# Optimization experiments

Measured on AMD Instinct MI355X. Metric: run time of the kernel, lower is better.

Reference implementation:

```python
import jax, jax.numpy as jnp
import numpy as np

B = 8192
NUM_SAMPLES = 128
RESAMPLE_PADDING = 0.01
F32_EPS = float(np.finfo(np.float32).eps)


def lift_gaussian_diag(d, t_mean, t_var, r_var):
    # d: [B,3]; t_mean/t_var/r_var: [B,S]
    mean = d[..., None, :] * t_mean[..., None]                      # [B,S,3]
    d_mag_sq = jnp.clip(jnp.sum(d ** 2, axis=-1, keepdims=True), 1e-10)
    d_outer_diag = d ** 2
    null_outer_diag = 1.0 - d_outer_diag / d_mag_sq
    cov_diag = (t_var[..., None] * d_outer_diag[..., None, :]
                + r_var[..., None] * null_outer_diag[..., None, :])  # [B,S,3]
    return mean, cov_diag


def conical_frustum_to_gaussian(d, t0, t1, base_radius):
    # stable=True branch of the original code
    mu = (t0 + t1) / 2
    hw = (t1 - t0) / 2
    t_mean = mu + 2 * mu * hw ** 2 / (3 * mu ** 2 + hw ** 2)
    t_var = hw ** 2 / 3 - 4 / 15 * (hw ** 4 * (12 * mu ** 2 - hw ** 2)
                                    / (3 * mu ** 2 + hw ** 2) ** 2)
    r_var = base_radius ** 2 * (mu ** 2 / 4 + 5 / 12 * hw ** 2
                                - 4 / 15 * hw ** 4 / (3 * mu ** 2 + hw ** 2))
    return lift_gaussian_diag(d, t_mean, t_var, r_var)


def cast_rays(t_vals, origins, directions, radii):
    # ray_shape == 'cone', diag == True
    means, covs = conical_frustum_to_gaussian(
        directions, t_vals[..., :-1], t_vals[..., 1:], radii)
    return means + origins[..., None, :], covs


def sorted_piecewise_constant_pdf(bins, weights, num_samples):
    # randomized=False branch; faithful O(n*m) mask-based interval search
    eps = 1e-5
    weight_sum = jnp.sum(weights, axis=-1, keepdims=True)
    padding = jnp.clip(eps - weight_sum, 0)
    weights = weights + padding / weights.shape[-1]
    weight_sum = weight_sum + padding
    pdf = weights / weight_sum
    cdf = jnp.minimum(jnp.cumsum(pdf[..., :-1], axis=-1), 1.0)
    z = jnp.zeros(cdf.shape[:-1] + (1,), cdf.dtype)
    o = jnp.ones(cdf.shape[:-1] + (1,), cdf.dtype)
    cdf = jnp.concatenate([z, cdf, o], axis=-1)                      # [B, nb+1]
    u = jnp.linspace(0.0, 1.0 - F32_EPS, num_samples, dtype=cdf.dtype)
    u = jnp.broadcast_to(u, cdf.shape[:-1] + (num_samples,))         # [B, S]
    mask = u[..., None, :] >= cdf[..., :, None]                      # [B, nb+1, S]

    def find_interval(x):
        x0 = jnp.max(jnp.where(mask, x[..., None], x[..., :1, None]), axis=-2)
        x1 = jnp.min(jnp.where(~mask, x[..., None], x[..., -1:, None]), axis=-2)
        return x0, x1

    bins_g0, bins_g1 = find_interval(bins)
    cdf_g0, cdf_g1 = find_interval(cdf)
    t = jnp.clip(jnp.nan_to_num((u - cdf_g0) / (cdf_g1 - cdf_g0)), 0, 1)
    return bins_g0 + t * (bins_g1 - bins_g0)


def setup_inputs() -> dict:
    key = jax.random.key(0)
    k0, k1, k2, k3 = jax.random.split(key, 4)
    origins = jax.random.normal(k0, (B, 3), dtype=jnp.float32)
    directions = jax.random.normal(k1, (B, 3), dtype=jnp.float32)
    directions = directions / jnp.linalg.norm(directions, axis=-1, keepdims=True)
    radii = 0.001 + 0.01 * jax.random.uniform(k2, (B, 1), dtype=jnp.float32)
    near = 2.0 * jnp.ones((B, 1), dtype=jnp.float32)
    far = 6.0 * jnp.ones((B, 1), dtype=jnp.float32)
    weights = jax.random.uniform(k3, (B, NUM_SAMPLES), dtype=jnp.float32)
    return {"origins": origins, "directions": directions, "radii": radii,
            "near": near, "far": far, "weights": weights}


def reference(origins, directions, radii, near, far, weights):
    # coarse stratified sampling (randomized=False, lindisp=False)
    t = jnp.linspace(0.0, 1.0, NUM_SAMPLES + 1, dtype=jnp.float32)
    t_coarse = near * (1.0 - t) + far * t                            # [B, S+1]
    means_c, covs_c = cast_rays(t_coarse, origins, directions, radii)
    # resample_along_rays: blur weights then inverse-CDF sample
    wpad = jnp.concatenate([weights[..., :1], weights, weights[..., -1:]], axis=-1)
    wmax = jnp.maximum(wpad[..., :-1], wpad[..., 1:])
    wblur = 0.5 * (wmax[..., :-1] + wmax[..., 1:]) + RESAMPLE_PADDING
    t_fine = sorted_piecewise_constant_pdf(t_coarse, wblur, t_coarse.shape[-1])
    means_f, covs_f = cast_rays(t_fine, origins, directions, radii)
    return (t_coarse, means_c, covs_c, t_fine, means_f, covs_f)
```

## Files before the change

kernel.cpp:

```cpp
#include <hip/hip_runtime.h>


constexpr int B_RAYS = 8192;
constexpr int S      = 128;
constexpr int SP1    = 129;
constexpr float F32_EPS = 1.1920928955078125e-07f;

constexpr long long O_TC = 0;
constexpr long long O_MC = O_TC + (long long)B_RAYS * SP1;
constexpr long long O_CC = O_MC + (long long)B_RAYS * S * 3;
constexpr long long O_TF = O_CC + (long long)B_RAYS * S * 3;
constexpr long long O_MF = O_TF + (long long)B_RAYS * SP1;
constexpr long long O_CF = O_MF + (long long)B_RAYS * S * 3;

__device__ __forceinline__ void cast_and_store(
    const float* __restrict__ sh_tv,
    float* __restrict__ sh_stage,
    float dx, float dy, float dz,
    float ox, float oy, float oz,
    float rad2, float dmag2,
    float* __restrict__ out_means,
    float* __restrict__ out_covs,
    int tid)
{
    float t0 = sh_tv[tid], t1 = sh_tv[tid + 1];
    float mu  = 0.5f * (t0 + t1);
    float hw  = 0.5f * (t1 - t0);
    float mu2 = mu * mu, hw2 = hw * hw, hw4 = hw2 * hw2;
    float den = 3.0f * mu2 + hw2;
    float t_mean = mu + (2.0f * mu * hw2) / den;
    float t_var  = hw2 * (1.0f / 3.0f)
                 - (4.0f / 15.0f) * ((hw4 * (12.0f * mu2 - hw2)) / (den * den));
    float r_var  = rad2 * (0.25f * mu2 + (5.0f / 12.0f) * hw2
                 - (4.0f / 15.0f) * (hw4 / den));

    float dxx = dx * dx, dyy = dy * dy, dzz = dz * dz;

    sh_stage[3 * tid + 0] = dx * t_mean + ox;
    sh_stage[3 * tid + 1] = dy * t_mean + oy;
    sh_stage[3 * tid + 2] = dz * t_mean + oz;
    sh_stage[384 + 3 * tid + 0] = t_var * dxx + r_var * (1.0f - dxx / dmag2);
    sh_stage[384 + 3 * tid + 1] = t_var * dyy + r_var * (1.0f - dyy / dmag2);
    sh_stage[384 + 3 * tid + 2] = t_var * dzz + r_var * (1.0f - dzz / dmag2);
    __syncthreads();
    #pragma unroll
    for (int j = 0; j < 3; ++j) {
        out_means[j * 128 + tid] = sh_stage[j * 128 + tid];
        out_covs [j * 128 + tid] = sh_stage[384 + j * 128 + tid];
    }
}

__global__ __launch_bounds__(128) void mipnerf_kernel(
    const float* __restrict__ origins,
    const float* __restrict__ directions,
    const float* __restrict__ radii,
    const float* __restrict__ nearp,
    const float* __restrict__ farp,
    const float* __restrict__ weights,
    float* __restrict__ out)
{
    const int b   = blockIdx.x;
    const int tid = threadIdx.x;

    __shared__ float sh_t[SP1];
    __shared__ float sh_tf[SP1];
    __shared__ float sh_cdf[SP1];
    __shared__ float sh_w[S];
    __shared__ float sh_stage[2 * S * 3];
    __shared__ float sh_red[2];
    __shared__ float sh_wavetot;

    const float ox = origins[3 * b], oy = origins[3 * b + 1], oz = origins[3 * b + 2];
    const float dx = directions[3 * b], dy = directions[3 * b + 1], dz = directions[3 * b + 2];
    const float rad  = radii[b];
    const float rad2 = rad * rad;
    const float nv = nearp[b], fv = farp[b];
    const float dmag2 = fmaxf(dx * dx + dy * dy + dz * dz, 1e-10f);

    for (int i = tid; i < SP1; i += 128) {
        float t  = (float)i * (1.0f / 128.0f);
        float tc = nv * (1.0f - t) + fv * t;
        sh_t[i] = tc;
        out[O_TC + (long long)b * SP1 + i] = tc;
    }
    sh_w[tid] = weights[(long long)b * S + tid];
    __syncthreads();

    cast_and_store(sh_t, sh_stage, dx, dy, dz, ox, oy, oz, rad2, dmag2,
                   out + O_MC + (long long)b * S * 3,
                   out + O_CC + (long long)b * S * 3, tid);

    float wi  = sh_w[tid];
    float wml = fmaxf((tid > 0     ? sh_w[tid - 1] : wi), wi);
    float wmr = fmaxf(wi, (tid < S - 1 ? sh_w[tid + 1] : wi));
    float wb  = 0.5f * (wml + wmr) + 0.01f;

    float v = wb;
    #pragma unroll
    for (int off = 32; off >= 1; off >>= 1) v += __shfl_down(v, off);
    if ((tid & 63) == 0) sh_red[tid >> 6] = v;
    __syncthreads();
    float wsum    = sh_red[0] + sh_red[1];
    float padding = fmaxf(1e-5f - wsum, 0.0f);
    float wstot   = wsum + padding;
    float pdf     = (wb + padding * (1.0f / (float)S)) / wstot;

    float x   = pdf;
    int lane  = tid & 63;
    #pragma unroll
    for (int off = 1; off < 64; off <<= 1) {
        float y = __shfl_up(x, off);
        if (lane >= off) x += y;
    }
    if (tid == 63) sh_wavetot = x;
    __syncthreads();
    if (tid >= 64) x += sh_wavetot;

    if (tid == 0) { sh_cdf[0] = 0.0f; sh_cdf[S] = 1.0f; }
    if (tid < S - 1) sh_cdf[tid + 1] = fminf(x, 1.0f);
    __syncthreads();

    const float ustep = (1.0f - F32_EPS) * (1.0f / 128.0f);
    for (int s = tid; s < SP1; s += 128) {
        float u = (float)s * ustep;
        int lo = 0, hi = S;
        #pragma unroll
        for (int it = 0; it < 7; ++it) {
            int mid = (lo + hi) >> 1;
            if (sh_cdf[mid] <= u) lo = mid; else hi = mid;
        }
        float cg0 = sh_cdf[lo], cg1 = sh_cdf[lo + 1];
        float bg0 = sh_t[lo],   bg1 = sh_t[lo + 1];
        float tt  = (u - cg0) / (cg1 - cg0);
        if (!(tt == tt)) tt = 0.0f;
        tt = fminf(fmaxf(tt, 0.0f), 1.0f);
        float tf = bg0 + tt * (bg1 - bg0);
        sh_tf[s] = tf;
        out[O_TF + (long long)b * SP1 + s] = tf;
    }
    __syncthreads();

    cast_and_store(sh_tf, sh_stage, dx, dy, dz, ox, oy, oz, rad2, dmag2,
                   out + O_MF + (long long)b * S * 3,
                   out + O_CF + (long long)b * S * 3, tid);
}

extern "C" void kernel_launch(void* const* d_in, const int* in_sizes, int n_in,
                              void* d_out, int out_size, void* d_ws, size_t ws_size,
                              hipStream_t stream)
{
    const float* origins    = (const float*)d_in[0];
    const float* directions = (const float*)d_in[1];
    const float* radii      = (const float*)d_in[2];
    const float* nearp      = (const float*)d_in[3];
    const float* farp       = (const float*)d_in[4];
    const float* weights    = (const float*)d_in[5];
    float* out = (float*)d_out;

    mipnerf_kernel<<<B_RAYS, 128, 0, stream>>>(
        origins, directions, radii, nearp, farp, weights, out);
}
```

Baseline: 21.30 us.

## Process one ray per wavefront, four rays per block, without block barriers

```diff
diff --git a/kernel.cpp b/kernel.cpp
--- a/kernel.cpp
+++ b/kernel.cpp
@@ -13,44 +13,26 @@
 constexpr long long O_MF = O_TF + (long long)B_RAYS * SP1;
 constexpr long long O_CF = O_MF + (long long)B_RAYS * S * 3;
 
-__device__ __forceinline__ void cast_and_store(
-    const float* __restrict__ sh_tv,
-    float* __restrict__ sh_stage,
-    float dx, float dy, float dz,
-    float ox, float oy, float oz,
-    float rad2, float dmag2,
-    float* __restrict__ out_means,
-    float* __restrict__ out_covs,
-    int tid)
+__device__ __forceinline__ void frustum(float t0, float t1, float rad2,
+                                        float& tm, float& tv, float& rv)
 {
-    float t0 = sh_tv[tid], t1 = sh_tv[tid + 1];
     float mu  = 0.5f * (t0 + t1);
     float hw  = 0.5f * (t1 - t0);
     float mu2 = mu * mu, hw2 = hw * hw, hw4 = hw2 * hw2;
     float den = 3.0f * mu2 + hw2;
-    float t_mean = mu + (2.0f * mu * hw2) / den;
-    float t_var  = hw2 * (1.0f / 3.0f)
-                 - (4.0f / 15.0f) * ((hw4 * (12.0f * mu2 - hw2)) / (den * den));
-    float r_var  = rad2 * (0.25f * mu2 + (5.0f / 12.0f) * hw2
-                 - (4.0f / 15.0f) * (hw4 / den));
-
-    float dxx = dx * dx, dyy = dy * dy, dzz = dz * dz;
-
-    sh_stage[3 * tid + 0] = dx * t_mean + ox;
-    sh_stage[3 * tid + 1] = dy * t_mean + oy;
-    sh_stage[3 * tid + 2] = dz * t_mean + oz;
-    sh_stage[384 + 3 * tid + 0] = t_var * dxx + r_var * (1.0f - dxx / dmag2);
-    sh_stage[384 + 3 * tid + 1] = t_var * dyy + r_var * (1.0f - dyy / dmag2);
-    sh_stage[384 + 3 * tid + 2] = t_var * dzz + r_var * (1.0f - dzz / dmag2);
-    __syncthreads();
-    #pragma unroll
-    for (int j = 0; j < 3; ++j) {
-        out_means[j * 128 + tid] = sh_stage[j * 128 + tid];
-        out_covs [j * 128 + tid] = sh_stage[384 + j * 128 + tid];
-    }
+    float rden = 1.0f / den;
+    tm = mu + (2.0f * mu * hw2) * rden;
+    tv = hw2 * (1.0f / 3.0f)
+       - (4.0f / 15.0f) * (hw4 * (12.0f * mu2 - hw2)) * (rden * rden);
+    rv = rad2 * (0.25f * mu2 + (5.0f / 12.0f) * hw2 - (4.0f / 15.0f) * hw4 * rden);
 }
 
-__global__ __launch_bounds__(128) void mipnerf_kernel(
+__device__ __forceinline__ float sel3(int c, float x, float y, float z)
+{
+    return (c == 0) ? x : ((c == 1) ? y : z);
+}
+
+__global__ __launch_bounds__(256) void mipnerf_kernel(
     const float* __restrict__ origins,
     const float* __restrict__ directions,
     const float* __restrict__ radii,
@@ -59,90 +41,124 @@
     const float* __restrict__ weights,
     float* __restrict__ out)
 {
-    const int b   = blockIdx.x;
     const int tid = threadIdx.x;
+    const int w   = tid >> 6;
+    const int l   = tid & 63;
+    const int b   = (blockIdx.x << 2) + w;
 
-    __shared__ float sh_t[SP1];
-    __shared__ float sh_tf[SP1];
-    __shared__ float sh_cdf[SP1];
-    __shared__ float sh_w[S];
-    __shared__ float sh_stage[2 * S * 3];
-    __shared__ float sh_red[2];
-    __shared__ float sh_wavetot;
+    __shared__ float s_tm[4][128];
+    __shared__ float s_tv[4][128];
+    __shared__ float s_rv[4][128];
+    __shared__ float s_cdf[4][132];
+    __shared__ float s_tf[4][132];
 
-    const float ox = origins[3 * b], oy = origins[3 * b + 1], oz = origins[3 * b + 2];
-    const float dx = directions[3 * b], dy = directions[3 * b + 1], dz = directions[3 * b + 2];
+    const float ox = origins[3*b+0], oy = origins[3*b+1], oz = origins[3*b+2];
+    const float dx = directions[3*b+0], dy = directions[3*b+1], dz = directions[3*b+2];
     const float rad  = radii[b];
     const float rad2 = rad * rad;
     const float nv = nearp[b], fv = farp[b];
-    const float dmag2 = fmaxf(dx * dx + dy * dy + dz * dz, 1e-10f);
+    const float dmag2 = fmaxf(dx*dx + dy*dy + dz*dz, 1e-10f);
+    const float axx = dx*dx, ayy = dy*dy, azz = dz*dz;
+    const float nxx = 1.0f - axx/dmag2, nyy = 1.0f - ayy/dmag2, nzz = 1.0f - azz/dmag2;
 
-    for (int i = tid; i < SP1; i += 128) {
-        float t  = (float)i * (1.0f / 128.0f);
-        float tc = nv * (1.0f - t) + fv * t;
-        sh_t[i] = tc;
-        out[O_TC + (long long)b * SP1 + i] = tc;
+    auto bin = [&](int k) {
+        float t = (float)k * (1.0f / 128.0f);
+        return nv * (1.0f - t) + fv * t;
+    };
+
+    auto write_cast = [&](float* __restrict__ om, float* __restrict__ oc) {
+        #pragma unroll
+        for (int j = 0; j < 3; ++j) {
+            int f0 = 2 * (l + 64*j);
+            int ia = f0 / 3,      ca = f0 - 3*ia;
+            int ib2 = (f0+1) / 3, cb = (f0+1) - 3*ib2;
+            float tma = s_tm[w][ia], tmb = s_tm[w][ib2];
+            float2 mv;
+            mv.x = sel3(ca, dx, dy, dz) * tma + sel3(ca, ox, oy, oz);
+            mv.y = sel3(cb, dx, dy, dz) * tmb + sel3(cb, ox, oy, oz);
+            *reinterpret_cast<float2*>(om + f0) = mv;
+            float2 cv;
+            cv.x = s_tv[w][ia] * sel3(ca, axx, ayy, azz)
+                 + s_rv[w][ia] * sel3(ca, nxx, nyy, nzz);
+            cv.y = s_tv[w][ib2] * sel3(cb, axx, ayy, azz)
+                 + s_rv[w][ib2] * sel3(cb, nxx, nyy, nzz);
+            *reinterpret_cast<float2*>(oc + f0) = cv;
+        }
+    };
+
+    for (int s = l; s < SP1; s += 64)
+        out[O_TC + (long long)b * SP1 + s] = bin(s);
+
+    #pragma unroll
+    for (int j = 0; j < 2; ++j) {
+        int i = l + 64*j;
+        float tm, tv, rv;
+        frustum(bin(i), bin(i+1), rad2, tm, tv, rv);
+        s_tm[w][i] = tm; s_tv[w][i] = tv; s_rv[w][i] = rv;
     }
-    sh_w[tid] = weights[(long long)b * S + tid];
-    __syncthreads();
+    __builtin_amdgcn_wave_barrier();
 
-    cast_and_store(sh_t, sh_stage, dx, dy, dz, ox, oy, oz, rad2, dmag2,
-                   out + O_MC + (long long)b * S * 3,
-                   out + O_CC + (long long)b * S * 3, tid);
+    write_cast(out + O_MC + (long long)b * 384, out + O_CC + (long long)b * 384);
+    __builtin_amdgcn_wave_barrier();
 
-    float wi  = sh_w[tid];
-    float wml = fmaxf((tid > 0     ? sh_w[tid - 1] : wi), wi);
-    float wmr = fmaxf(wi, (tid < S - 1 ? sh_w[tid + 1] : wi));
-    float wb  = 0.5f * (wml + wmr) + 0.01f;
+    float2 wv = *reinterpret_cast<const float2*>(weights + (long long)b * S + 2*l);
+    float wprev = __shfl_up(wv.y, 1);   if (l == 0)  wprev = wv.x;
+    float wnext = __shfl_down(wv.x, 1); if (l == 63) wnext = wv.y;
+    float m0 = fmaxf(wprev, wv.x), m1 = fmaxf(wv.x, wv.y), m2 = fmaxf(wv.y, wnext);
+    float wb0 = 0.5f * (m0 + m1) + 0.01f;
+    float wb1 = 0.5f * (m1 + m2) + 0.01f;
 
-    float v = wb;
-    #pragma unroll
-    for (int off = 32; off >= 1; off >>= 1) v += __shfl_down(v, off);
-    if ((tid & 63) == 0) sh_red[tid >> 6] = v;
-    __syncthreads();
-    float wsum    = sh_red[0] + sh_red[1];
-    float padding = fmaxf(1e-5f - wsum, 0.0f);
-    float wstot   = wsum + padding;
-    float pdf     = (wb + padding * (1.0f / (float)S)) / wstot;
-
-    float x   = pdf;
-    int lane  = tid & 63;
+    float ps   = wb0 + wb1;
+    float incl = ps;
     #pragma unroll
     for (int off = 1; off < 64; off <<= 1) {
-        float y = __shfl_up(x, off);
-        if (lane >= off) x += y;
+        float y = __shfl_up(incl, off);
+        if (l >= off) incl += y;
     }
-    if (tid == 63) sh_wavetot = x;
-    __syncthreads();
-    if (tid >= 64) x += sh_wavetot;
+    float total = __shfl(incl, 63);
+    float pad   = fmaxf(1e-5f - total, 0.0f);
+    float wstot = total + pad;
+    float inv   = 1.0f / wstot;
+    float padk  = pad * (1.0f / 128.0f);
+    float excl  = incl - ps;
 
-    if (tid == 0) { sh_cdf[0] = 0.0f; sh_cdf[S] = 1.0f; }
-    if (tid < S - 1) sh_cdf[tid + 1] = fminf(x, 1.0f);
-    __syncthreads();
+    float c1 = fminf((excl + wb0 + (float)(2*l + 1) * padk) * inv, 1.0f);
+    float c2 = fminf((incl        + (float)(2*l + 2) * padk) * inv, 1.0f);
+    s_cdf[w][2*l + 1] = c1;
+    s_cdf[w][2*l + 2] = (l == 63) ? 1.0f : c2;
+    if (l == 0) s_cdf[w][0] = 0.0f;
+    __builtin_amdgcn_wave_barrier();
 
     const float ustep = (1.0f - F32_EPS) * (1.0f / 128.0f);
-    for (int s = tid; s < SP1; s += 128) {
+    for (int s = l; s < SP1; s += 64) {
         float u = (float)s * ustep;
-        int lo = 0, hi = S;
+        int lo = 0, hi = 128;
         #pragma unroll
         for (int it = 0; it < 7; ++it) {
             int mid = (lo + hi) >> 1;
-            if (sh_cdf[mid] <= u) lo = mid; else hi = mid;
+            if (s_cdf[w][mid] <= u) lo = mid; else hi = mid;
         }
-        float cg0 = sh_cdf[lo], cg1 = sh_cdf[lo + 1];
-        float bg0 = sh_t[lo],   bg1 = sh_t[lo + 1];
-        float tt  = (u - cg0) / (cg1 - cg0);
+        float c0  = s_cdf[w][lo], cg1 = s_cdf[w][lo + 1];
+        float tt  = (u - c0) / (cg1 - c0);
         if (!(tt == tt)) tt = 0.0f;
         tt = fminf(fmaxf(tt, 0.0f), 1.0f);
-        float tf = bg0 + tt * (bg1 - bg0);
-        sh_tf[s] = tf;
+        float b0  = bin(lo);
+        float tf  = b0 + tt * (bin(lo + 1) - b0);
+        s_tf[w][s] = tf;
         out[O_TF + (long long)b * SP1 + s] = tf;
     }
-    __syncthreads();
+    __builtin_amdgcn_wave_barrier();
 
-    cast_and_store(sh_tf, sh_stage, dx, dy, dz, ox, oy, oz, rad2, dmag2,
-                   out + O_MF + (long long)b * S * 3,
-                   out + O_CF + (long long)b * S * 3, tid);
+    #pragma unroll
+    for (int j = 0; j < 2; ++j) {
+        int i = l + 64*j;
+        float tm, tv, rv;
+        frustum(s_tf[w][i], s_tf[w][i+1], rad2, tm, tv, rv);
+        s_tm[w][i] = tm; s_tv[w][i] = tv; s_rv[w][i] = rv;
+    }
+    __builtin_amdgcn_wave_barrier();
+
+    write_cast(out + O_MF + (long long)b * 384, out + O_CF + (long long)b * 384);
 }
 
 extern "C" void kernel_launch(void* const* d_in, const int* in_sizes, int n_in,
@@ -157,6 +173,6 @@
     const float* weights    = (const float*)d_in[5];
     float* out = (float*)d_out;
 
-    mipnerf_kernel<<<B_RAYS, 128, 0, stream>>>(
+    mipnerf_kernel<<<B_RAYS / 4, 256, 0, stream>>>(
         origins, directions, radii, nearp, farp, weights, out);
 }
```

Result: faster. 19.64 us (-7.8%).
